# Optimization experiments

Measured on AMD Instinct MI355X. Metric: run time of the kernel, lower is better.

## Reference

```python
import jax, jax.numpy as jnp
import numpy as np

D_MODEL = 16
D_FF = 32
BLOCK = 64
B = 16384
EPS = 1e-5


def setup_inputs() -> dict:
    key = jax.random.key(0)
    ks = jax.random.split(key, 8)
    s = 1.0 / np.sqrt(D_MODEL)
    return {
        "x": jax.random.normal(ks[0], (B, BLOCK, D_MODEL), dtype=jnp.float32),
        # attention projections, stored as [in, out] so y = x @ W
        "Wk": jax.random.uniform(ks[1], (D_MODEL, D_MODEL), jnp.float32, -s, s),
        "Wq": jax.random.uniform(ks[2], (D_MODEL, D_MODEL), jnp.float32, -s, s),
        "Wv": jax.random.uniform(ks[3], (D_MODEL, D_MODEL), jnp.float32, -s, s),
        "ln1_g": jnp.ones((D_MODEL,), jnp.float32),
        "ln1_b": jnp.zeros((D_MODEL,), jnp.float32),
        "ln2_g": jnp.ones((D_MODEL,), jnp.float32),
        "ln2_b": jnp.zeros((D_MODEL,), jnp.float32),
        "W1": jax.random.uniform(ks[4], (D_MODEL, D_FF), jnp.float32, -s, s),
        "b1": jax.random.uniform(ks[5], (D_FF,), jnp.float32, -s, s),
        "W2": jax.random.uniform(ks[6], (D_FF, D_MODEL), jnp.float32, -1/np.sqrt(D_FF), 1/np.sqrt(D_FF)),
        "b2": jax.random.uniform(ks[7], (D_MODEL,), jnp.float32, -1/np.sqrt(D_FF), 1/np.sqrt(D_FF)),
    }


def _layernorm(x, g, b):
    mu = jnp.mean(x, axis=-1, keepdims=True)
    var = jnp.mean(jnp.square(x - mu), axis=-1, keepdims=True)
    return (x - mu) * jax.lax.rsqrt(var + EPS) * g + b


def reference(x, Wk, Wq, Wv, ln1_g, ln1_b, ln2_g, ln2_b, W1, b1, W2, b2):
    B_, T, C = x.shape
    h = _layernorm(x, ln1_g, ln1_b)
    k = h @ Wk
    q = h @ Wq
    v = h @ Wv
    att = jnp.einsum("btc,bsc->bts", q, k) / jnp.sqrt(jnp.float32(C))
    causal = jnp.tril(jnp.ones((T, T), dtype=bool))
    att = jnp.where(causal, att, -jnp.inf)
    att = jax.nn.softmax(att, axis=-1)
    y = jnp.einsum("bts,bsc->btc", att, v)
    x = x + y
    h2 = _layernorm(x, ln2_g, ln2_b)
    ff = jax.nn.gelu(h2 @ W1 + b1, approximate=False) @ W2 + b2
    return x + ff
```

## Files before the change

kernel.cpp:

```cpp
#include <hip/hip_runtime.h>
#include <hip/hip_bf16.h>


typedef __attribute__((ext_vector_type(4))) short bf4;
typedef __attribute__((ext_vector_type(4))) float f4;

union Frag2 { uint2 u2; uint u[2]; bf4 b; };
union F4U  { uint4 u4; float4 f; };

__device__ __forceinline__ uint packbf(float lo, float hi) {
    union { __hip_bfloat162 h; uint u; } c;
    c.h = __float22bfloat162_rn(make_float2(lo, hi));
    return c.u;
}

__device__ __forceinline__ float gelu_fast(float u) {
    float u2 = u * u;
    float t  = u * (-2.3022079f + -0.1029431f * u2);
    float e  = __builtin_amdgcn_exp2f(t);
    return u * __builtin_amdgcn_rcpf(1.f + e);
}

#define MFMA16(a, b, c) __builtin_amdgcn_mfma_f32_16x16x16bf16_1k(a, b, c, 0, 0, 0)

#define NWAVES 4

#define WS_SLOTS 16

__device__ __forceinline__ uint2 wfrag16(const float* __restrict__ W, int ld,
                                         int n, int q, float s) {
    uint2 w;
    w.x = packbf(W[(q*4+0)*ld+n]*s, W[(q*4+1)*ld+n]*s);
    w.y = packbf(W[(q*4+2)*ld+n]*s, W[(q*4+3)*ld+n]*s);
    return w;
}

__global__ __launch_bounds__(64, 1)
void prep_kernel(const float* __restrict__ Wk, const float* __restrict__ Wq,
                 const float* __restrict__ Wv,
                 const float* __restrict__ ln1g, const float* __restrict__ ln1b,
                 const float* __restrict__ ln2g, const float* __restrict__ ln2b,
                 const float* __restrict__ W1, const float* __restrict__ b1,
                 const float* __restrict__ W2, const float* __restrict__ b2,
                 uint4* __restrict__ ws)
{
    const int lane = threadIdx.x;
    const int c15  = lane & 15;
    const int quad = lane >> 4;
    const int quad4 = quad << 2;
    uint4* o = ws + lane * WS_SLOTS;
    uint2 fq  = wfrag16(Wq, 16, c15, quad, 0.25f*1.44269504f);
    uint2 fk  = wfrag16(Wk, 16, c15, quad, 1.0f);
    uint2 fv  = wfrag16(Wv, 16, c15, quad, 1.0f);
    uint2 f1a = wfrag16(W1, 32, c15,      quad, 1.0f);
    uint2 f1b = wfrag16(W1, 32, c15 + 16, quad, 1.0f);
    uint2 f2a = wfrag16(W2,        16, c15, quad, 1.0f);
    uint2 f2b = wfrag16(W2 + 256,  16, c15, quad, 1.0f);
    o[0] = make_uint4(fq.x, fq.y, fk.x, fk.y);
    o[1] = make_uint4(fv.x, fv.y, f1a.x, f1a.y);
    o[2] = make_uint4(f1b.x, f1b.y, f2a.x, f2a.y);
    o[3] = make_uint4(f2b.x, f2b.y, 0u, 0u);
    F4U a;
    a.f = *(const float4*)(ln1g + quad4); o[4]  = a.u4;
    a.f = *(const float4*)(ln1b + quad4); o[5]  = a.u4;
    a.f = *(const float4*)(ln2g + quad4); o[6]  = a.u4;
    a.f = *(const float4*)(ln2b + quad4); o[7]  = a.u4;
    a.f = *(const float4*)(b1 + quad4);      o[8]  = a.u4;
    a.f = *(const float4*)(b1 + 16 + quad4); o[9]  = a.u4;
    a.f = *(const float4*)(b2 + quad4);      o[10] = a.u4;
}

__global__ __launch_bounds__(64 * NWAVES, 4)
void tb_kernel(const float* __restrict__ x,
               const uint4* __restrict__ ws,
               float* __restrict__ out)
{
    const int tid  = threadIdx.x;
    const int lane = tid & 63;
    const int wid  = tid >> 6;
    const int c15  = lane & 15;
    const int quad = lane >> 4;
    const int quad4 = quad << 2;
    const size_t base = (size_t)(blockIdx.x * NWAVES + wid) * (64 * 16);
    const f4 z4 = {0.f, 0.f, 0.f, 0.f};

    float4 xr[4];
    #pragma unroll
    for (int qt = 0; qt < 4; ++qt)
        xr[qt] = *(const float4*)(x + base + (size_t)(qt*16 + c15)*16 + quad4);

    const uint4* wv = ws + lane * WS_SLOTS;
    uint4 s0 = wv[0], s1 = wv[1], s2 = wv[2], s3 = wv[3];
    Frag2 T;
    T.u[0]=s0.x; T.u[1]=s0.y; const bf4 fWq  = T.b;
    T.u[0]=s0.z; T.u[1]=s0.w; const bf4 fWk  = T.b;
    T.u[0]=s1.x; T.u[1]=s1.y; const bf4 fWv  = T.b;
    T.u[0]=s1.z; T.u[1]=s1.w; const bf4 fW1a = T.b;
    T.u[0]=s2.x; T.u[1]=s2.y; const bf4 fW1b = T.b;
    T.u[0]=s2.z; T.u[1]=s2.w; const bf4 fW2a = T.b;
    T.u[0]=s3.x; T.u[1]=s3.y; const bf4 fW2b = T.b;
    F4U fu;
    fu.u4 = wv[4];  const float4 g1  = fu.f;
    fu.u4 = wv[5];  const float4 b1l = fu.f;
    fu.u4 = wv[6];  const float4 g2  = fu.f;
    fu.u4 = wv[7];  const float4 b2l = fu.f;
    fu.u4 = wv[8];  const f4 cb0 = {fu.f.x, fu.f.y, fu.f.z, fu.f.w};
    fu.u4 = wv[9];  const f4 cb1 = {fu.f.x, fu.f.y, fu.f.z, fu.f.w};
    fu.u4 = wv[10]; const f4 cb2 = {fu.f.x, fu.f.y, fu.f.z, fu.f.w};

    bf4 idf;
    {
        const int d = c15 - quad4;
        Frag2 I_;
        I_.u[0] = (d == 0) ? 0x00003F80u : (d == 1) ? 0x3F800000u : 0u;
        I_.u[1] = (d == 2) ? 0x00003F80u : (d == 3) ? 0x3F800000u : 0u;
        idf = I_.b;
    }

    bf4 ah[4];
    #pragma unroll
    for (int qt = 0; qt < 4; ++qt) {
        float4 v = xr[qt];
        float s = v.x + v.y + v.z + v.w;
        s += __shfl_xor(s, 16); s += __shfl_xor(s, 32);
        float mu = s * 0.0625f;
        float d0 = v.x-mu, d1 = v.y-mu, d2 = v.z-mu, d3 = v.w-mu;
        float s2 = d0*d0 + d1*d1 + d2*d2 + d3*d3;
        s2 += __shfl_xor(s2, 16); s2 += __shfl_xor(s2, 32);
        float rstd = rsqrtf(s2 * 0.0625f + 1e-5f);
        float h0 = d0*rstd*g1.x + b1l.x;
        float h1 = d1*rstd*g1.y + b1l.y;
        float h2 = d2*rstd*g1.z + b1l.z;
        float h3 = d3*rstd*g1.w + b1l.w;
        Frag2 A; A.u[0] = packbf(h0, h1); A.u[1] = packbf(h2, h3);
        ah[qt] = A.b;
    }

    bf4 va[4], ka[4], qb[4];
    #pragma unroll
    for (int mt = 0; mt < 4; ++mt) {
        f4 qc = MFMA16(ah[mt], fWq, z4);
        f4 kc = MFMA16(ah[mt], fWk, z4);
        f4 vc = MFMA16(ah[mt], fWv, z4);
        Frag2 Aq, Ak, V_;
        Aq.u[0] = packbf(qc[0], qc[1]); Aq.u[1] = packbf(qc[2], qc[3]);
        Ak.u[0] = packbf(kc[0], kc[1]); Ak.u[1] = packbf(kc[2], kc[3]);
        V_.u[0] = packbf(vc[0], vc[1]); V_.u[1] = packbf(vc[2], vc[3]);
        va[mt] = V_.b;
        f4 tq = MFMA16(Aq.b, idf, z4);
        f4 tk = MFMA16(Ak.b, idf, z4);
        Frag2 Qb, Ka;
        Qb.u[0] = packbf(tq[0], tq[1]); Qb.u[1] = packbf(tq[2], tq[3]);
        Ka.u[0] = packbf(tk[0], tk[1]); Ka.u[1] = packbf(tk[2], tk[3]);
        qb[mt] = Qb.b;
        ka[mt] = Ka.b;
    }

    f4 st[4][4];
    #pragma unroll
    for (int kt = 0; kt < 4; ++kt)
        #pragma unroll
        for (int qt = 3; qt >= 0; --qt)
            if (qt >= kt)
                st[kt][qt] = MFMA16(ka[kt], qb[qt], z4);
    #pragma unroll
    for (int qt = 0; qt < 4; ++qt)
        #pragma unroll
        for (int r = 0; r < 4; ++r)
            st[qt][qt][r] = (quad4 + r <= c15) ? st[qt][qt][r] : -1e30f;

    float linv[4];
    #pragma unroll
    for (int qt = 0; qt < 4; ++qt) {
        float l = 0.f;
        #pragma unroll
        for (int kt = 0; kt < 4; ++kt) {
            if (kt <= qt) {
                #pragma unroll
                for (int r = 0; r < 4; ++r) {
                    float p = __builtin_amdgcn_exp2f(st[kt][qt][r]);
                    st[kt][qt][r] = p;
                    l += p;
                }
            }
        }
        l += __shfl_xor(l, 16);
        l += __shfl_xor(l, 32);
        linv[qt] = __builtin_amdgcn_rcpf(l);
    }

    f4 yt[4];
    #pragma unroll
    for (int qt = 0; qt < 4; ++qt) {
        f4 acc = z4;
        #pragma unroll
        for (int kt = 0; kt < 4; ++kt) {
            if (kt <= qt) {
                Frag2 P_;
                P_.u[0] = packbf(st[kt][qt][0], st[kt][qt][1]);
                P_.u[1] = packbf(st[kt][qt][2], st[kt][qt][3]);
                acc = MFMA16(va[kt], P_.b, acc);
            }
        }
        yt[qt] = acc;
    }

    float x2v[4][4];
    f4 uu0[4], uu1[4];
    #pragma unroll
    for (int qt = 0; qt < 4; ++qt) {
        const float li = linv[qt];
        x2v[qt][0] = xr[qt].x + yt[qt][0]*li;
        x2v[qt][1] = xr[qt].y + yt[qt][1]*li;
        x2v[qt][2] = xr[qt].z + yt[qt][2]*li;
        x2v[qt][3] = xr[qt].w + yt[qt][3]*li;
        float s = x2v[qt][0]+x2v[qt][1]+x2v[qt][2]+x2v[qt][3];
        s += __shfl_xor(s, 16); s += __shfl_xor(s, 32);
        float mu = s * 0.0625f;
        float d0 = x2v[qt][0]-mu, d1 = x2v[qt][1]-mu,
              d2 = x2v[qt][2]-mu, d3 = x2v[qt][3]-mu;
        float s2 = d0*d0 + d1*d1 + d2*d2 + d3*d3;
        s2 += __shfl_xor(s2, 16); s2 += __shfl_xor(s2, 32);
        float rstd = rsqrtf(s2 * 0.0625f + 1e-5f);
        float h0 = d0*rstd*g2.x + b2l.x;
        float h1 = d1*rstd*g2.y + b2l.y;
        float h2 = d2*rstd*g2.z + b2l.z;
        float h3 = d3*rstd*g2.w + b2l.w;
        Frag2 Hb;
        Hb.u[0] = packbf(h0, h1); Hb.u[1] = packbf(h2, h3);
        uu0[qt] = MFMA16(fW1a, Hb.b, cb0);
        uu1[qt] = MFMA16(fW1b, Hb.b, cb1);
    }
    #pragma unroll
    for (int qt = 0; qt < 4; ++qt) {
        Frag2 Pa, Pb;
        Pa.u[0] = packbf(gelu_fast(uu0[qt][0]), gelu_fast(uu0[qt][1]));
        Pa.u[1] = packbf(gelu_fast(uu0[qt][2]), gelu_fast(uu0[qt][3]));
        Pb.u[0] = packbf(gelu_fast(uu1[qt][0]), gelu_fast(uu1[qt][1]));
        Pb.u[1] = packbf(gelu_fast(uu1[qt][2]), gelu_fast(uu1[qt][3]));
        f4 fo = MFMA16(fW2a, Pa.b, cb2);
        fo = MFMA16(fW2b, Pb.b, fo);
        float4 o;
        o.x = x2v[qt][0] + fo[0];
        o.y = x2v[qt][1] + fo[1];
        o.z = x2v[qt][2] + fo[2];
        o.w = x2v[qt][3] + fo[3];
        *(float4*)(out + base + (size_t)(qt*16 + c15)*16 + quad4) = o;
    }
}

extern "C" void kernel_launch(void* const* d_in, const int* in_sizes, int n_in,
                              void* d_out, int out_size, void* d_ws, size_t ws_size,
                              hipStream_t stream) {
    const float* x     = (const float*)d_in[0];
    const float* Wk    = (const float*)d_in[1];
    const float* Wq    = (const float*)d_in[2];
    const float* Wv    = (const float*)d_in[3];
    const float* ln1_g = (const float*)d_in[4];
    const float* ln1_b = (const float*)d_in[5];
    const float* ln2_g = (const float*)d_in[6];
    const float* ln2_b = (const float*)d_in[7];
    const float* W1    = (const float*)d_in[8];
    const float* b1    = (const float*)d_in[9];
    const float* W2    = (const float*)d_in[10];
    const float* b2    = (const float*)d_in[11];
    float* out = (float*)d_out;
    uint4* ws = (uint4*)d_ws;

    prep_kernel<<<1, 64, 0, stream>>>(Wk, Wq, Wv, ln1_g, ln1_b, ln2_g, ln2_b,
                                      W1, b1, W2, b2, ws);
    const int n_blocks = in_sizes[0] / (64 * 16);
    const int nwg = n_blocks / NWAVES;
    tb_kernel<<<nwg, 64 * NWAVES, 0, stream>>>(x, ws, out);
}
```

Baseline: 148.9 us.

## Drop identity-MFMA transposes and process two blocks per wave

Q and K are now computed already transposed by swapping MFMA operand order, using the weight fragment as the A operand. This removes the identity-matrix MFMA pass and its extra bf16 repacking. Each wave now handles two 64-token blocks, halving the grid, which amortises weight-fragment loads and gives more independent work per wave. The score, softmax and PV stages are fused per query tile, with probabilities packed to bf16 immediately, to cut live registers. Doubling the per-wave state risks higher register pressure and fewer resident waves.

```diff
diff --git a/kernel.cpp b/kernel.cpp
--- a/kernel.cpp
+++ b/kernel.cpp
@@ -24,6 +24,7 @@
 #define MFMA16(a, b, c) __builtin_amdgcn_mfma_f32_16x16x16bf16_1k(a, b, c, 0, 0, 0)
 
 #define NWAVES 4
+#define BLKW 2
 
 #define WS_SLOTS 16
 
@@ -81,13 +82,17 @@
     const int c15  = lane & 15;
     const int quad = lane >> 4;
     const int quad4 = quad << 2;
-    const size_t base = (size_t)(blockIdx.x * NWAVES + wid) * (64 * 16);
+    const size_t blk0 = ((size_t)blockIdx.x * NWAVES + wid) * BLKW;
     const f4 z4 = {0.f, 0.f, 0.f, 0.f};
 
-    float4 xr[4];
-    #pragma unroll
-    for (int qt = 0; qt < 4; ++qt)
-        xr[qt] = *(const float4*)(x + base + (size_t)(qt*16 + c15)*16 + quad4);
+    float4 xr[BLKW][4];
+    #pragma unroll
+    for (int b = 0; b < BLKW; ++b) {
+        const float* xb = x + (blk0 + b) * 1024;
+        #pragma unroll
+        for (int qt = 0; qt < 4; ++qt)
+            xr[b][qt] = *(const float4*)(xb + (size_t)(qt*16 + c15)*16 + quad4);
+    }
 
     const uint4* wv = ws + lane * WS_SLOTS;
     uint4 s0 = wv[0], s1 = wv[1], s2 = wv[2], s3 = wv[3];
@@ -108,19 +113,12 @@
     fu.u4 = wv[9];  const f4 cb1 = {fu.f.x, fu.f.y, fu.f.z, fu.f.w};
     fu.u4 = wv[10]; const f4 cb2 = {fu.f.x, fu.f.y, fu.f.z, fu.f.w};
 
-    bf4 idf;
-    {
-        const int d = c15 - quad4;
-        Frag2 I_;
-        I_.u[0] = (d == 0) ? 0x00003F80u : (d == 1) ? 0x3F800000u : 0u;
-        I_.u[1] = (d == 2) ? 0x00003F80u : (d == 3) ? 0x3F800000u : 0u;
-        idf = I_.b;
-    }
-
-    bf4 ah[4];
+    bf4 ah[BLKW][4];
+    #pragma unroll
+    for (int b = 0; b < BLKW; ++b)
     #pragma unroll
     for (int qt = 0; qt < 4; ++qt) {
-        float4 v = xr[qt];
+        float4 v = xr[b][qt];
         float s = v.x + v.y + v.z + v.w;
         s += __shfl_xor(s, 16); s += __shfl_xor(s, 32);
         float mu = s * 0.0625f;
@@ -133,119 +131,101 @@
         float h2 = d2*rstd*g1.z + b1l.z;
         float h3 = d3*rstd*g1.w + b1l.w;
         Frag2 A; A.u[0] = packbf(h0, h1); A.u[1] = packbf(h2, h3);
-        ah[qt] = A.b;
+        ah[b][qt] = A.b;
     }
 
-    bf4 va[4], ka[4], qb[4];
-    #pragma unroll
-    for (int mt = 0; mt < 4; ++mt) {
-        f4 qc = MFMA16(ah[mt], fWq, z4);
-        f4 kc = MFMA16(ah[mt], fWk, z4);
-        f4 vc = MFMA16(ah[mt], fWv, z4);
-        Frag2 Aq, Ak, V_;
-        Aq.u[0] = packbf(qc[0], qc[1]); Aq.u[1] = packbf(qc[2], qc[3]);
-        Ak.u[0] = packbf(kc[0], kc[1]); Ak.u[1] = packbf(kc[2], kc[3]);
-        V_.u[0] = packbf(vc[0], vc[1]); V_.u[1] = packbf(vc[2], vc[3]);
-        va[mt] = V_.b;
-        f4 tq = MFMA16(Aq.b, idf, z4);
-        f4 tk = MFMA16(Ak.b, idf, z4);
-        Frag2 Qb, Ka;
-        Qb.u[0] = packbf(tq[0], tq[1]); Qb.u[1] = packbf(tq[2], tq[3]);
-        Ka.u[0] = packbf(tk[0], tk[1]); Ka.u[1] = packbf(tk[2], tk[3]);
-        qb[mt] = Qb.b;
-        ka[mt] = Ka.b;
-    }
-
-    f4 st[4][4];
-    #pragma unroll
-    for (int kt = 0; kt < 4; ++kt)
-        #pragma unroll
-        for (int qt = 3; qt >= 0; --qt)
-            if (qt >= kt)
-                st[kt][qt] = MFMA16(ka[kt], qb[qt], z4);
-    #pragma unroll
-    for (int qt = 0; qt < 4; ++qt)
-        #pragma unroll
-        for (int r = 0; r < 4; ++r)
-            st[qt][qt][r] = (quad4 + r <= c15) ? st[qt][qt][r] : -1e30f;
-
-    float linv[4];
-    #pragma unroll
-    for (int qt = 0; qt < 4; ++qt) {
-        float l = 0.f;
-        #pragma unroll
-        for (int kt = 0; kt < 4; ++kt) {
-            if (kt <= qt) {
-                #pragma unroll
-                for (int r = 0; r < 4; ++r) {
-                    float p = __builtin_amdgcn_exp2f(st[kt][qt][r]);
-                    st[kt][qt][r] = p;
-                    l += p;
-                }
+    #pragma unroll
+    for (int b = 0; b < BLKW; ++b) {
+        bf4 qb[4], ka[4], va[4];
+        #pragma unroll
+        for (int mt = 0; mt < 4; ++mt) {
+            f4 tq = MFMA16(fWq, ah[b][mt], z4);
+            f4 tk = MFMA16(fWk, ah[b][mt], z4);
+            f4 vc = MFMA16(ah[b][mt], fWv, z4);
+            Frag2 Qb, Ka, V_;
+            Qb.u[0] = packbf(tq[0], tq[1]); Qb.u[1] = packbf(tq[2], tq[3]);
+            Ka.u[0] = packbf(tk[0], tk[1]); Ka.u[1] = packbf(tk[2], tk[3]);
+            V_.u[0] = packbf(vc[0], vc[1]); V_.u[1] = packbf(vc[2], vc[3]);
+            qb[mt] = Qb.b; ka[mt] = Ka.b; va[mt] = V_.b;
+        }
+
+        uint2 pk[4][4];
+        float linv[4];
+        #pragma unroll
+        for (int qt = 0; qt < 4; ++qt) {
+            f4 stc[4];
+            #pragma unroll
+            for (int kt = 0; kt <= qt; ++kt)
+                stc[kt] = MFMA16(ka[kt], qb[qt], z4);
+            #pragma unroll
+            for (int r = 0; r < 4; ++r)
+                stc[qt][r] = (quad4 + r <= c15) ? stc[qt][r] : -1e30f;
+            float l = 0.f;
+            #pragma unroll
+            for (int kt = 0; kt <= qt; ++kt) {
+                float p0 = __builtin_amdgcn_exp2f(stc[kt][0]);
+                float p1 = __builtin_amdgcn_exp2f(stc[kt][1]);
+                float p2 = __builtin_amdgcn_exp2f(stc[kt][2]);
+                float p3 = __builtin_amdgcn_exp2f(stc[kt][3]);
+                l += (p0 + p1) + (p2 + p3);
+                pk[kt][qt] = make_uint2(packbf(p0, p1), packbf(p2, p3));
             }
-        }
-        l += __shfl_xor(l, 16);
-        l += __shfl_xor(l, 32);
-        linv[qt] = __builtin_amdgcn_rcpf(l);
-    }
-
-    f4 yt[4];
-    #pragma unroll
-    for (int qt = 0; qt < 4; ++qt) {
-        f4 acc = z4;
-        #pragma unroll
-        for (int kt = 0; kt < 4; ++kt) {
-            if (kt <= qt) {
+            l += __shfl_xor(l, 16);
+            l += __shfl_xor(l, 32);
+            linv[qt] = __builtin_amdgcn_rcpf(l);
+        }
+
+        float x2v[4][4];
+        f4 uu0[4], uu1[4];
+        #pragma unroll
+        for (int qt = 0; qt < 4; ++qt) {
+            f4 acc = z4;
+            #pragma unroll
+            for (int kt = 0; kt <= qt; ++kt) {
                 Frag2 P_;
-                P_.u[0] = packbf(st[kt][qt][0], st[kt][qt][1]);
-                P_.u[1] = packbf(st[kt][qt][2], st[kt][qt][3]);
+                P_.u2 = pk[kt][qt];
                 acc = MFMA16(va[kt], P_.b, acc);
             }
-        }
-        yt[qt] = acc;
-    }
-
-    float x2v[4][4];
-    f4 uu0[4], uu1[4];
-    #pragma unroll
-    for (int qt = 0; qt < 4; ++qt) {
-        const float li = linv[qt];
-        x2v[qt][0] = xr[qt].x + yt[qt][0]*li;
-        x2v[qt][1] = xr[qt].y + yt[qt][1]*li;
-        x2v[qt][2] = xr[qt].z + yt[qt][2]*li;
-        x2v[qt][3] = xr[qt].w + yt[qt][3]*li;
-        float s = x2v[qt][0]+x2v[qt][1]+x2v[qt][2]+x2v[qt][3];
-        s += __shfl_xor(s, 16); s += __shfl_xor(s, 32);
-        float mu = s * 0.0625f;
-        float d0 = x2v[qt][0]-mu, d1 = x2v[qt][1]-mu,
-              d2 = x2v[qt][2]-mu, d3 = x2v[qt][3]-mu;
-        float s2 = d0*d0 + d1*d1 + d2*d2 + d3*d3;
-        s2 += __shfl_xor(s2, 16); s2 += __shfl_xor(s2, 32);
-        float rstd = rsqrtf(s2 * 0.0625f + 1e-5f);
-        float h0 = d0*rstd*g2.x + b2l.x;
-        float h1 = d1*rstd*g2.y + b2l.y;
-        float h2 = d2*rstd*g2.z + b2l.z;
-        float h3 = d3*rstd*g2.w + b2l.w;
-        Frag2 Hb;
-        Hb.u[0] = packbf(h0, h1); Hb.u[1] = packbf(h2, h3);
-        uu0[qt] = MFMA16(fW1a, Hb.b, cb0);
-        uu1[qt] = MFMA16(fW1b, Hb.b, cb1);
-    }
-    #pragma unroll
-    for (int qt = 0; qt < 4; ++qt) {
-        Frag2 Pa, Pb;
-        Pa.u[0] = packbf(gelu_fast(uu0[qt][0]), gelu_fast(uu0[qt][1]));
-        Pa.u[1] = packbf(gelu_fast(uu0[qt][2]), gelu_fast(uu0[qt][3]));
-        Pb.u[0] = packbf(gelu_fast(uu1[qt][0]), gelu_fast(uu1[qt][1]));
-        Pb.u[1] = packbf(gelu_fast(uu1[qt][2]), gelu_fast(uu1[qt][3]));
-        f4 fo = MFMA16(fW2a, Pa.b, cb2);
-        fo = MFMA16(fW2b, Pb.b, fo);
-        float4 o;
-        o.x = x2v[qt][0] + fo[0];
-        o.y = x2v[qt][1] + fo[1];
-        o.z = x2v[qt][2] + fo[2];
-        o.w = x2v[qt][3] + fo[3];
-        *(float4*)(out + base + (size_t)(qt*16 + c15)*16 + quad4) = o;
+            const float li = linv[qt];
+            x2v[qt][0] = xr[b][qt].x + acc[0]*li;
+            x2v[qt][1] = xr[b][qt].y + acc[1]*li;
+            x2v[qt][2] = xr[b][qt].z + acc[2]*li;
+            x2v[qt][3] = xr[b][qt].w + acc[3]*li;
+            float s = x2v[qt][0]+x2v[qt][1]+x2v[qt][2]+x2v[qt][3];
+            s += __shfl_xor(s, 16); s += __shfl_xor(s, 32);
+            float mu = s * 0.0625f;
+            float d0 = x2v[qt][0]-mu, d1 = x2v[qt][1]-mu,
+                  d2 = x2v[qt][2]-mu, d3 = x2v[qt][3]-mu;
+            float s2 = d0*d0 + d1*d1 + d2*d2 + d3*d3;
+            s2 += __shfl_xor(s2, 16); s2 += __shfl_xor(s2, 32);
+            float rstd = rsqrtf(s2 * 0.0625f + 1e-5f);
+            float h0 = d0*rstd*g2.x + b2l.x;
+            float h1 = d1*rstd*g2.y + b2l.y;
+            float h2 = d2*rstd*g2.z + b2l.z;
+            float h3 = d3*rstd*g2.w + b2l.w;
+            Frag2 Hb;
+            Hb.u[0] = packbf(h0, h1); Hb.u[1] = packbf(h2, h3);
+            uu0[qt] = MFMA16(fW1a, Hb.b, cb0);
+            uu1[qt] = MFMA16(fW1b, Hb.b, cb1);
+        }
+
+        float* ob = out + (blk0 + b) * 1024;
+        #pragma unroll
+        for (int qt = 0; qt < 4; ++qt) {
+            Frag2 Pa, Pb;
+            Pa.u[0] = packbf(gelu_fast(uu0[qt][0]), gelu_fast(uu0[qt][1]));
+            Pa.u[1] = packbf(gelu_fast(uu0[qt][2]), gelu_fast(uu0[qt][3]));
+            Pb.u[0] = packbf(gelu_fast(uu1[qt][0]), gelu_fast(uu1[qt][1]));
+            Pb.u[1] = packbf(gelu_fast(uu1[qt][2]), gelu_fast(uu1[qt][3]));
+            f4 fo = MFMA16(fW2a, Pa.b, cb2);
+            fo = MFMA16(fW2b, Pb.b, fo);
+            float4 o;
+            o.x = x2v[qt][0] + fo[0];
+            o.y = x2v[qt][1] + fo[1];
+            o.z = x2v[qt][2] + fo[2];
+            o.w = x2v[qt][3] + fo[3];
+            *(float4*)(ob + (size_t)(qt*16 + c15)*16 + quad4) = o;
+        }
     }
 }
 
@@ -270,6 +250,6 @@
     prep_kernel<<<1, 64, 0, stream>>>(Wk, Wq, Wv, ln1_g, ln1_b, ln2_g, ln2_b,
                                       W1, b1, W2, b2, ws);
     const int n_blocks = in_sizes[0] / (64 * 16);
-    const int nwg = n_blocks / NWAVES;
+    const int nwg = n_blocks / (NWAVES * BLKW);
     tb_kernel<<<nwg, 64 * NWAVES, 0, stream>>>(x, ws, out);
 }
```

Result: slower. 156.7 us (+5.3%).
